# Kernel tuning notes

Measured on AMD Instinct MI355X. Metric: run time of the kernel, lower is better.

The kernel has to match this reference:

```python
import jax, jax.numpy as jnp
import numpy as np
from jax import lax

H, W = 4096, 4096

def setup_inputs() -> dict:
    key = jax.random.key(0)
    k_occ, k_seed = jax.random.split(key)
    occupied = (jax.random.uniform(k_occ, (H, W)) < 0.3).astype(jnp.float32)
    flood = ((jax.random.uniform(k_seed, (H, W)) < 1e-3).astype(jnp.float32)
             * (1.0 - occupied))
    flood_input = jnp.stack([occupied, flood], axis=-1)  # [H, W, 2]
    flood_count = jnp.zeros((H, W), dtype=jnp.float32)
    # Fixed flood kernel, HWIO layout: (3, 3, in=2, out=1)
    kernel = jnp.zeros((3, 3, 2, 1), dtype=jnp.float32)
    kernel = kernel.at[1, 1, 0, 0].set(-5.0)  # occupied center blocks flood
    kernel = kernel.at[1, 2, 1, 0].set(1.0)   # right
    kernel = kernel.at[2, 1, 1, 0].set(1.0)   # down
    kernel = kernel.at[1, 0, 1, 0].set(1.0)   # left
    kernel = kernel.at[0, 1, 1, 0].set(1.0)   # up
    kernel = kernel.at[1, 1, 1, 0].set(1.0)   # center
    bias = jnp.zeros((1,), dtype=jnp.float32)
    return {"flood_input": flood_input, "flood_count": flood_count,
            "kernel": kernel, "bias": bias, "num_steps": 16}

def reference(flood_input, flood_count, kernel, bias, num_steps):
    dn = ("NHWC", "HWIO", "NHWC")

    def flood_step(carry, _):
        x, count = carry                      # x: [H, W, 2], count: [H, W]
        occupied = x[..., 0]
        y = lax.conv_general_dilated(x[None], kernel, (1, 1), "SAME",
                                     dimension_numbers=dn)[0, ..., 0] + bias[0]
        y = jnp.clip(y, 0.0, 1.0)             # flooded frontier
        new_x = jnp.stack([occupied, y], axis=-1)
        return (new_x, count + y), None

    (x_final, count_final), _ = lax.scan(flood_step,
                                         (flood_input, flood_count),
                                         None, length=num_steps)
    # [H, W, 3]: occupied, flood, count
    return jnp.concatenate([x_final, count_final[..., None]], axis=-1)
```

## Files before the change

kernel.cpp:

```cpp
#include <hip/hip_runtime.h>


typedef unsigned long long u64;
typedef float f32x4 __attribute__((ext_vector_type(4)));
typedef float f32x2 __attribute__((ext_vector_type(2)));

#define HH 4096
#define WW 4096
#define WPR 64
#define NSTEPS 16
#define HALO 16
#define IT 32

__global__ __launch_bounds__(256) void pack_kernel(
    const float* __restrict__ flood_input,
    u64* __restrict__ occP, u64* __restrict__ flP)
{
    const int lane = threadIdx.x & 63;
    const int wv   = threadIdx.x >> 6;
    const int r    = blockIdx.x;
#pragma unroll
    for (int b = 0; b < 2; ++b) {
        float vx[8], vy[8];
#pragma unroll
        for (int j = 0; j < 8; ++j) {
            const int w = wv * 16 + b * 8 + j;
            const f32x2 v = __builtin_nontemporal_load(
                (const f32x2*)(flood_input +
                                ((size_t)r * WW + (w << 6) + lane) * 2));
            vx[j] = v[0]; vy[j] = v[1];
        }
#pragma unroll
        for (int j = 0; j < 8; ++j) {
            const int w = wv * 16 + b * 8 + j;
            const u64 om = __ballot(vx[j] > 0.5f);
            const u64 fm = __ballot(vy[j] > 0.5f);
            if (lane == 0) {
                occP[(size_t)r * WPR + w] = om;
                flP [(size_t)r * WPR + w] = fm;
            }
        }
    }
}

__global__ __launch_bounds__(256, 8) void flood_kernel(
    const u64* __restrict__ occP, const u64* __restrict__ flP,
    const float* __restrict__ flood_count,
    float* __restrict__ out)
{
    __shared__ u64 plane[4][IT][7];
    __shared__ float out2[4][2 * 128 * 3];

    const int tid  = threadIdx.x;
    const int lane = tid & 63;
    const int wv   = tid >> 6;

    const int wgid = blockIdx.y * 32 + blockIdx.x;
    const int nl   = (wgid & 7) * 512 + (wgid >> 3);
    const int bx   = nl & 31;
    const int by   = nl >> 5;

    const int tile_r0 = by * IT;
    const int tile_c0 = bx * (4 * IT) + wv * IT;
    const int bc0     = bx * (4 * IT);

    const int gr  = tile_r0 - HALO + lane;
    const bool rin = (gr >= 0) & (gr < HH);
    const int s   = tile_c0 - HALO;
    const int q0  = ((s + 64) >> 6) - 1;
    const int sh  = s - (q0 << 6);

    const size_t base = (size_t)(rin ? gr : 0) * WPR;
    const int qa = min(max(q0, 0), WPR - 1);
    const int qb = min(max(q0 + 1, 0), WPR - 1);
    u64 o0 = occP[base + qa], o1 = occP[base + qb];
    u64 f0 = flP [base + qa], f1 = flP [base + qb];
    const bool va = rin & (q0 >= 0);
    const bool vb = rin & (q0 + 1 < WPR);
    if (!va) { o0 = ~0ull; f0 = 0ull; }
    if (!vb) { o1 = ~0ull; f1 = 0ull; }
    const u64 occ = (o0 >> sh) | (sh ? (o1 << (64 - sh)) : 0ull);
    u64       f   = (f0 >> sh) | (sh ? (f1 << (64 - sh)) : 0ull);

    const int half = lane >> 5;
    const int l32  = lane & 31;
    const int col0 = l32 * 4;
    const float* fcbase = flood_count +
        (size_t)(tile_r0 + wv * 8 + half) * WW + bc0 + col0;
    f32x4 fc_next = __builtin_nontemporal_load((const f32x4*)fcbase);

    const u64 nocc = ~occ;
    u64 c0 = 0, c1 = 0, c2 = 0, c3 = 0, c4 = 0;
#pragma unroll
    for (int it = 0; it < NSTEPS; ++it) {
        u64 up = __shfl_up(f, 1);
        u64 dn = __shfl_down(f, 1);
        if (lane == 0)  up = 0ull;
        if (lane == 63) dn = 0ull;
        f = nocc & (f | (f << 1) | (f >> 1) | up | dn);
        u64 c = f, t;
        t = c0; c0 = t ^ c; c = t & c;
        t = c1; c1 = t ^ c; c = t & c;
        t = c2; c2 = t ^ c; c = t & c;
        t = c3; c3 = t ^ c; c = t & c;
        c4 ^= c;
    }

    if (lane >= HALO && lane < HALO + IT) {
        u64* p = plane[wv][lane - HALO];
        p[0] = occ; p[1] = f;
        p[2] = c0; p[3] = c1; p[4] = c2; p[5] = c3; p[6] = c4;
    }
    __syncthreads();

    const int sw   = col0 >> 5;
    const int bit0 = HALO + (col0 & 31);
    for (int t = 0; t < 4; ++t) {
        const f32x4 fc4 = fc_next;
        if (t + 1 < 4)
            fc_next = __builtin_nontemporal_load(
                (const f32x4*)(fcbase + (size_t)(t + 1) * 2 * WW));

        const int rA   = wv * 8 + 2 * t;
        const int irow = rA + half;
        const u64* p = plane[sw][irow];
        const u64 ow = p[0], fw = p[1];
        const u64 k0 = p[2], k1 = p[3], k2 = p[4], k3 = p[5], k4 = p[6];

        float v[12];
#pragma unroll
        for (int j = 0; j < 4; ++j) {
            const int bit = bit0 + j;
            int cv = (int)((k0 >> bit) & 1ull)
                   + ((int)((k1 >> bit) & 1ull) << 1)
                   + ((int)((k2 >> bit) & 1ull) << 2)
                   + ((int)((k3 >> bit) & 1ull) << 3)
                   + ((int)((k4 >> bit) & 1ull) << 4);
            v[j*3+0] = (float)((ow >> bit) & 1ull);
            v[j*3+1] = (float)((fw >> bit) & 1ull);
            v[j*3+2] = (float)cv + fc4[j];
        }
        float* dst = &out2[wv][half * 384 + l32 * 12];
        *(f32x4*)(dst + 0) = (f32x4){v[0], v[1], v[2],  v[3]};
        *(f32x4*)(dst + 4) = (f32x4){v[4], v[5], v[6],  v[7]};
        *(f32x4*)(dst + 8) = (f32x4){v[8], v[9], v[10], v[11]};

        __syncthreads();

#pragma unroll
        for (int st = 0; st < 3; ++st) {
            const int L   = st * 256 + lane * 4;
            const int row = (L >= 384) ? 1 : 0;
            const int off = L - row * 384;
            const f32x4 q = *(const f32x4*)(&out2[wv][L]);
            __builtin_nontemporal_store(q,
                (f32x4*)(out + ((size_t)(tile_r0 + rA + row) * WW + bc0) * 3
                         + off));
        }
    }
}

extern "C" void kernel_launch(void* const* d_in, const int* in_sizes, int n_in,
                              void* d_out, int out_size, void* d_ws, size_t ws_size,
                              hipStream_t stream) {
    const float* flood_input = (const float*)d_in[0];
    const float* flood_cnt   = (const float*)d_in[1];
    float* out = (float*)d_out;

    u64* occP = (u64*)d_ws;
    u64* flP  = occP + (size_t)HH * WPR;

    pack_kernel<<<dim3(HH), dim3(256), 0, stream>>>(flood_input, occP, flP);

    dim3 grid(WW / (4 * IT), HH / IT);
    flood_kernel<<<grid, dim3(256), 0, stream>>>(occP, flP, flood_cnt, out);
}
```

Baseline: 357.7 us.

## Fuse pack and flood kernels into one cooperative launch with grid sync

Merges the bit-packing pass and the flood pass into a single persistent cooperative kernel of 2048 workgroups. Each workgroup first packs two rows, then waits at a grid-wide barrier and processes two flood tiles. This removes the second kernel launch and the gap between the kernels. The cost is a grid barrier and a fixed-size grid, which limits occupancy, and the two-kernel path is kept as a fallback if the cooperative launch fails.

```diff
diff --git a/kernel.cpp b/kernel.cpp
--- a/kernel.cpp
+++ b/kernel.cpp
@@ -1,5 +1,8 @@
 #include <hip/hip_runtime.h>
-
+#include <hip/hip_cooperative_groups.h>
+
+
+namespace cg = cooperative_groups;
 
 typedef unsigned long long u64;
 typedef float f32x4 __attribute__((ext_vector_type(4)));
@@ -12,57 +15,13 @@
 #define HALO 16
 #define IT 32
 
-__global__ __launch_bounds__(256) void pack_kernel(
-    const float* __restrict__ flood_input,
-    u64* __restrict__ occP, u64* __restrict__ flP)
-{
-    const int lane = threadIdx.x & 63;
-    const int wv   = threadIdx.x >> 6;
-    const int r    = blockIdx.x;
-#pragma unroll
-    for (int b = 0; b < 2; ++b) {
-        float vx[8], vy[8];
-#pragma unroll
-        for (int j = 0; j < 8; ++j) {
-            const int w = wv * 16 + b * 8 + j;
-            const f32x2 v = __builtin_nontemporal_load(
-                (const f32x2*)(flood_input +
-                                ((size_t)r * WW + (w << 6) + lane) * 2));
-            vx[j] = v[0]; vy[j] = v[1];
-        }
-#pragma unroll
-        for (int j = 0; j < 8; ++j) {
-            const int w = wv * 16 + b * 8 + j;
-            const u64 om = __ballot(vx[j] > 0.5f);
-            const u64 fm = __ballot(vy[j] > 0.5f);
-            if (lane == 0) {
-                occP[(size_t)r * WPR + w] = om;
-                flP [(size_t)r * WPR + w] = fm;
-            }
-        }
-    }
-}
-
-__global__ __launch_bounds__(256, 8) void flood_kernel(
+__device__ __forceinline__ void flood_tile(
     const u64* __restrict__ occP, const u64* __restrict__ flP,
-    const float* __restrict__ flood_count,
-    float* __restrict__ out)
-{
-    __shared__ u64 plane[4][IT][7];
-    __shared__ float out2[4][2 * 128 * 3];
-
-    const int tid  = threadIdx.x;
-    const int lane = tid & 63;
-    const int wv   = tid >> 6;
-
-    const int wgid = blockIdx.y * 32 + blockIdx.x;
-    const int nl   = (wgid & 7) * 512 + (wgid >> 3);
-    const int bx   = nl & 31;
-    const int by   = nl >> 5;
-
-    const int tile_r0 = by * IT;
-    const int tile_c0 = bx * (4 * IT) + wv * IT;
-    const int bc0     = bx * (4 * IT);
+    const float* __restrict__ flood_count, float* __restrict__ out,
+    u64* __restrict__ planeBuf , float* __restrict__ out2Buf ,
+    int tile_r0, int bc0, int lane, int wv)
+{
+    const int tile_c0 = bc0 + wv * IT;
 
     const int gr  = tile_r0 - HALO + lane;
     const bool rin = (gr >= 0) & (gr < HH);
@@ -107,7 +66,7 @@
     }
 
     if (lane >= HALO && lane < HALO + IT) {
-        u64* p = plane[wv][lane - HALO];
+        u64* p = planeBuf + ((size_t)wv * IT + (lane - HALO)) * 7;
         p[0] = occ; p[1] = f;
         p[2] = c0; p[3] = c1; p[4] = c2; p[5] = c3; p[6] = c4;
     }
@@ -115,6 +74,7 @@
 
     const int sw   = col0 >> 5;
     const int bit0 = HALO + (col0 & 31);
+    float* out2w = out2Buf + wv * 768;
     for (int t = 0; t < 4; ++t) {
         const f32x4 fc4 = fc_next;
         if (t + 1 < 4)
@@ -123,7 +83,7 @@
 
         const int rA   = wv * 8 + 2 * t;
         const int irow = rA + half;
-        const u64* p = plane[sw][irow];
+        const u64* p = planeBuf + ((size_t)sw * IT + irow) * 7;
         const u64 ow = p[0], fw = p[1];
         const u64 k0 = p[2], k1 = p[3], k2 = p[4], k3 = p[5], k4 = p[6];
 
@@ -140,7 +100,7 @@
             v[j*3+1] = (float)((fw >> bit) & 1ull);
             v[j*3+2] = (float)cv + fc4[j];
         }
-        float* dst = &out2[wv][half * 384 + l32 * 12];
+        float* dst = out2w + half * 384 + l32 * 12;
         *(f32x4*)(dst + 0) = (f32x4){v[0], v[1], v[2],  v[3]};
         *(f32x4*)(dst + 4) = (f32x4){v[4], v[5], v[6],  v[7]};
         *(f32x4*)(dst + 8) = (f32x4){v[8], v[9], v[10], v[11]};
@@ -152,12 +112,119 @@
             const int L   = st * 256 + lane * 4;
             const int row = (L >= 384) ? 1 : 0;
             const int off = L - row * 384;
-            const f32x4 q = *(const f32x4*)(&out2[wv][L]);
+            const f32x4 q = *(const f32x4*)(out2w + L);
             __builtin_nontemporal_store(q,
                 (f32x4*)(out + ((size_t)(tile_r0 + rA + row) * WW + bc0) * 3
                          + off));
         }
     }
+}
+
+__global__ __launch_bounds__(256, 8) void fused_kernel(
+    const float* __restrict__ flood_input,
+    const float* __restrict__ flood_count,
+    u64* __restrict__ occP, u64* __restrict__ flP,
+    float* __restrict__ out)
+{
+    __shared__ u64   plane[4 * IT * 7];
+    __shared__ float out2 [4 * 768];
+
+    const int tid  = threadIdx.x;
+    const int lane = tid & 63;
+    const int wv   = tid >> 6;
+
+    const int wgid = blockIdx.x;
+    const int nl   = (wgid & 7) * 256 + (wgid >> 3);
+
+    {
+        const int prow  = 2 * nl + (wv >> 1);
+        const int wbase = (wv & 1) * 32;
+        const float* rp = flood_input + (size_t)prow * WW * 2;
+#pragma unroll
+        for (int b = 0; b < 8; ++b) {
+            float vx[4], vy[4];
+#pragma unroll
+            for (int j = 0; j < 4; ++j) {
+                const int w = wbase + b * 4 + j;
+                const f32x2 v = __builtin_nontemporal_load(
+                    (const f32x2*)(rp + ((w << 6) + lane) * 2));
+                vx[j] = v[0]; vy[j] = v[1];
+            }
+#pragma unroll
+            for (int j = 0; j < 4; ++j) {
+                const int w = wbase + b * 4 + j;
+                const u64 om = __ballot(vx[j] > 0.5f);
+                const u64 fm = __ballot(vy[j] > 0.5f);
+                if (lane == 0) {
+                    occP[(size_t)prow * WPR + w] = om;
+                    flP [(size_t)prow * WPR + w] = fm;
+                }
+            }
+        }
+    }
+
+    cg::this_grid().sync();
+
+    const int by  = nl >> 4;
+    const int bx0 = (2 * nl) & 31;
+    const int tile_r0 = by * IT;
+#pragma unroll 1
+    for (int tt = 0; tt < 2; ++tt) {
+        const int bc0 = (bx0 + tt) * (4 * IT);
+        flood_tile(occP, flP, flood_count, out, plane, out2,
+                   tile_r0, bc0, lane, wv);
+    }
+}
+
+__global__ __launch_bounds__(256) void pack_kernel(
+    const float* __restrict__ flood_input,
+    u64* __restrict__ occP, u64* __restrict__ flP)
+{
+    const int lane = threadIdx.x & 63;
+    const int wv   = threadIdx.x >> 6;
+    const int r    = blockIdx.x;
+#pragma unroll
+    for (int b = 0; b < 2; ++b) {
+        float vx[8], vy[8];
+#pragma unroll
+        for (int j = 0; j < 8; ++j) {
+            const int w = wv * 16 + b * 8 + j;
+            const f32x2 v = __builtin_nontemporal_load(
+                (const f32x2*)(flood_input +
+                                ((size_t)r * WW + (w << 6) + lane) * 2));
+            vx[j] = v[0]; vy[j] = v[1];
+        }
+#pragma unroll
+        for (int j = 0; j < 8; ++j) {
+            const int w = wv * 16 + b * 8 + j;
+            const u64 om = __ballot(vx[j] > 0.5f);
+            const u64 fm = __ballot(vy[j] > 0.5f);
+            if (lane == 0) {
+                occP[(size_t)r * WPR + w] = om;
+                flP [(size_t)r * WPR + w] = fm;
+            }
+        }
+    }
+}
+
+__global__ __launch_bounds__(256, 8) void flood_kernel(
+    const u64* __restrict__ occP, const u64* __restrict__ flP,
+    const float* __restrict__ flood_count,
+    float* __restrict__ out)
+{
+    __shared__ u64   plane[4 * IT * 7];
+    __shared__ float out2 [4 * 768];
+
+    const int lane = threadIdx.x & 63;
+    const int wv   = threadIdx.x >> 6;
+
+    const int wgid = blockIdx.y * 32 + blockIdx.x;
+    const int nl   = (wgid & 7) * 512 + (wgid >> 3);
+    const int bx   = nl & 31;
+    const int by   = nl >> 5;
+
+    flood_tile(occP, flP, flood_count, out, plane, out2,
+               by * IT, bx * (4 * IT), lane, wv);
 }
 
 extern "C" void kernel_launch(void* const* d_in, const int* in_sizes, int n_in,
@@ -170,8 +237,14 @@
     u64* occP = (u64*)d_ws;
     u64* flP  = occP + (size_t)HH * WPR;
 
-    pack_kernel<<<dim3(HH), dim3(256), 0, stream>>>(flood_input, occP, flP);
-
-    dim3 grid(WW / (4 * IT), HH / IT);
-    flood_kernel<<<grid, dim3(256), 0, stream>>>(occP, flP, flood_cnt, out);
-}
+    void* args[] = { (void*)&flood_input, (void*)&flood_cnt,
+                     (void*)&occP, (void*)&flP, (void*)&out };
+    const hipError_t e = hipLaunchCooperativeKernel(
+        (void*)fused_kernel, dim3(2048), dim3(256), args, 0, stream);
+
+    if (e != hipSuccess) {
+        pack_kernel<<<dim3(HH), dim3(256), 0, stream>>>(flood_input, occP, flP);
+        dim3 grid(WW / (4 * IT), HH / IT);
+        flood_kernel<<<grid, dim3(256), 0, stream>>>(occP, flP, flood_cnt, out);
+    }
+}
```

Result: slower. 666.2 us (+86.2%).
